# Optimization experiments

Hardware: AMD Instinct MI355X
Metric: run time of the kernel (lower is better)

Reference implementation:

```python
import jax, jax.numpy as jnp
import numpy as np

D = 48


def setup_inputs() -> dict:
    key = jax.random.key(0)
    k1, k2, k3, k4, k5 = jax.random.split(key, 5)
    B, N, d = 4, 512, D
    x = jax.random.normal(k1, (B, N, d), dtype=jnp.float32)
    # Linear(2d, 2d) and Linear(2d, d); stored as (in, out) so y = x @ W + b
    s1 = 1.0 / np.sqrt(2 * d)
    W1 = jax.random.uniform(k2, (2 * d, 2 * d), dtype=jnp.float32, minval=-s1, maxval=s1)
    b1 = jax.random.uniform(k3, (2 * d,), dtype=jnp.float32, minval=-s1, maxval=s1)
    W2 = jax.random.uniform(k4, (2 * d, d), dtype=jnp.float32, minval=-s1, maxval=s1)
    b2 = jax.random.uniform(k5, (d,), dtype=jnp.float32, minval=-s1, maxval=s1)
    return {"x": x, "W1": W1, "b1": b1, "W2": W2, "b2": b2}


def reference(x, W1, b1, W2, b2):
    B, N, d = x.shape
    # pairwise concat: [B, N, N, 2d] with (i, j) = (x_i, x_j)
    xi = jnp.broadcast_to(x[:, :, None, :], (B, N, N, d))
    xj = jnp.broadcast_to(x[:, None, :, :], (B, N, N, d))
    cat = jnp.concatenate([xi, xj], axis=-1)
    h = jax.nn.gelu(cat @ W1 + b1, approximate=False)  # torch GELU is exact erf form
    p = h @ W2 + b2  # [B, N, N, d]
    mask = jnp.triu(jnp.ones((N, N), dtype=bool), 1)  # j > i masked
    p = jnp.where(mask[None, :, :, None], 0.0, p)
    w = jnp.sqrt(jnp.sum(p * p, axis=-1))  # frobenius norm over feature dim -> [B, N, N]
    w = jnp.where(mask[None, :, :], -1e9, w)
    w = jax.nn.softmax(w, axis=-1)[..., None]  # softmax over j
    return jnp.sum(w * p, axis=2)  # [B, N, d]
```

## Files before the change

kernel.cpp:

```cpp
#include <hip/hip_runtime.h>
#include <hip/hip_bf16.h>
#include <hip/hip_fp16.h>
#include <math.h>

#define DD 48
#define NN 512
#define TWO_D 96
#define ROWS 2048
#define W2P 104

typedef __attribute__((ext_vector_type(8))) _Float16 f16x8;
typedef __attribute__((ext_vector_type(4))) float f32x4;
typedef __attribute__((ext_vector_type(2))) float f32x2;
typedef __attribute__((ext_vector_type(4))) unsigned int u32x4;

__device__ __forceinline__ __half2 h2cast(unsigned int u) { return __builtin_bit_cast(__half2, u); }

__device__ __forceinline__ f32x2 gelu_poly2(f32x2 u) {
    f32x2 lim;  lim  = 3.5777f;
    f32x2 nlim; nlim = -3.5777f;
    const f32x2 uc = __builtin_elementwise_min(__builtin_elementwise_max(u, nlim), lim);
    const f32x2 v = uc * uc;
    f32x2 c5; c5 = -1.04448e-6f;
    f32x2 c4; c4 = 4.61896e-5f;
    f32x2 c3; c3 = -8.62284e-4f;
    f32x2 c2; c2 = 9.22138e-3f;
    f32x2 c1; c1 = -6.58353e-2f;
    f32x2 c0; c0 = 3.98855e-1f;
    f32x2 E = __builtin_elementwise_fma(v, c5, c4);
    E = __builtin_elementwise_fma(v, E, c3);
    E = __builtin_elementwise_fma(v, E, c2);
    E = __builtin_elementwise_fma(v, E, c1);
    E = __builtin_elementwise_fma(v, E, c0);
    f32x2 hlf; hlf = 0.5f;
    return u * __builtin_elementwise_fma(uc, E, hlf);
}

__global__ __launch_bounds__(256) void precompute_kernel(
        const float* __restrict__ x,
        const float* __restrict__ W1,
        const float* __restrict__ b1,
        const float* __restrict__ W2,
        __half* __restrict__ Aout,
        __half* __restrict__ Bout,
        __half* __restrict__ W2T) {
    if (blockIdx.x == ROWS / 4) {
        for (int idx = threadIdx.x; idx < DD * TWO_D; idx += 256) {
            const int f = idx / TWO_D;
            const int k = idx - f * TWO_D;
            W2T[idx] = __float2half(W2[k * DD + f]);
        }
        return;
    }
    const int wave = threadIdx.x >> 6;
    const int lane = threadIdx.x & 63;
    const int row = blockIdx.x * 4 + wave;
    __shared__ float xs[4][DD];
    if (threadIdx.x < 4 * DD)
        xs[threadIdx.x / DD][threadIdx.x % DD] = x[blockIdx.x * 4 * DD + threadIdx.x];
    __syncthreads();
    for (int t = lane; t < TWO_D; t += 64) {
        float a0 = 0.f, a1 = 0.f;
#pragma unroll 8
        for (int k = 0; k < DD; ++k) {
            const float xv = xs[wave][k];
            a0 = fmaf(xv, W1[k * TWO_D + t], a0);
            a1 = fmaf(xv, W1[(DD + k) * TWO_D + t], a1);
        }
        Aout[row * TWO_D + t] = __float2half(a0 + b1[t]);
        Bout[row * TWO_D + t] = __float2half(a1);
    }
}


#define LOAD_PB(PB_, PTR_)                                                      \
  { _Pragma("unroll")                                                           \
    for (int ks = 0; ks < 3; ++ks)                                              \
      PB_[ks] = *(const u32x4*)&(PTR_)[ks * 32 + q8]; }

#define STREAM_KS(PB_, ACC_, PF_, NPTR_, KS_)                                   \
  { const u32x4 aw = avp[KS_];                                                  \
    const u32x4 bw = PB_[KS_];                                                  \
    if (PF_) PB_[KS_] = *(const u32x4*)&(NPTR_)[(KS_) * 32 + q8];               \
    const __half2 u0 = __hadd2(h2cast(aw.x), h2cast(bw.x));                     \
    const __half2 u1 = __hadd2(h2cast(aw.y), h2cast(bw.y));                     \
    const __half2 u2 = __hadd2(h2cast(aw.z), h2cast(bw.z));                     \
    const __half2 u3 = __hadd2(h2cast(aw.w), h2cast(bw.w));                     \
    f32x2 f0, f1, f2, f3;                                                       \
    { float2 t_ = __half22float2(u0); f0.x = t_.x; f0.y = t_.y; }               \
    { float2 t_ = __half22float2(u1); f1.x = t_.x; f1.y = t_.y; }               \
    { float2 t_ = __half22float2(u2); f2.x = t_.x; f2.y = t_.y; }               \
    { float2 t_ = __half22float2(u3); f3.x = t_.x; f3.y = t_.y; }               \
    const f32x2 g0 = gelu_poly2(f0);                                            \
    const f32x2 g1 = gelu_poly2(f1);                                            \
    const f32x2 g2 = gelu_poly2(f2);                                            \
    const f32x2 g3 = gelu_poly2(f3);                                            \
    union { f16x8 v; __half2 h2[4]; } hf;                                       \
    hf.h2[0] = __float22half2_rn(make_float2(g0.x, g0.y));                      \
    hf.h2[1] = __float22half2_rn(make_float2(g1.x, g1.y));                      \
    hf.h2[2] = __float22half2_rn(make_float2(g2.x, g2.y));                      \
    hf.h2[3] = __float22half2_rn(make_float2(g3.x, g3.y));                      \
    ACC_[0] = __builtin_amdgcn_mfma_f32_16x16x32_f16(bf0, hf.v, ACC_[0], 0, 0, 0); \
    ACC_[1] = __builtin_amdgcn_mfma_f32_16x16x32_f16(bf1, hf.v, ACC_[1], 0, 0, 0); \
    ACC_[2] = __builtin_amdgcn_mfma_f32_16x16x32_f16(bf2, hf.v, ACC_[2], 0, 0, 0); \
  }

#define FUSED_KS(PBa_, ACCa_, PFa_, NPa_, DOB_, PBb_, ACCb_, PFb_, NPb_)        \
  { _Pragma("unroll")                                                           \
    for (int ksi = 0; ksi < 3; ++ksi) {                                         \
      const f16x8 bf0 = *(const f16x8*)&w2s[(0 * 16 + n) * W2P + ksi * 32 + q8];\
      const f16x8 bf1 = *(const f16x8*)&w2s[(1 * 16 + n) * W2P + ksi * 32 + q8];\
      const f16x8 bf2 = *(const f16x8*)&w2s[(2 * 16 + n) * W2P + ksi * 32 + q8];\
      STREAM_KS(PBa_, ACCa_, PFa_, NPa_, ksi);                                  \
      if (DOB_) STREAM_KS(PBb_, ACCb_, PFb_, NPb_, ksi);                        \
    } }

#define CHUNK_EPI(J0_, I_, ACC_, L_, O_)                                        \
  { f32x2 pv[3][2];                                                             \
    f32x2 ss2; ss2 = 0.f;                                                       \
    _Pragma("unroll")                                                           \
    for (int t = 0; t < 3; ++t) {                                               \
      pv[t][0].x = ACC_[t][0]; pv[t][0].y = ACC_[t][1];                         \
      pv[t][1].x = ACC_[t][2]; pv[t][1].y = ACC_[t][3];                         \
      ss2 = __builtin_elementwise_fma(pv[t][0], pv[t][0], ss2);                 \
      ss2 = __builtin_elementwise_fma(pv[t][1], pv[t][1], ss2);                 \
    }                                                                           \
    float ss = ss2.x + ss2.y;                                                   \
    ss += __shfl_xor(ss, 16);                                                   \
    ss += __shfl_xor(ss, 32);                                                   \
    const int j = (J0_) + n;                                                    \
    const float ew = (j <= (I_))                                                \
        ? __builtin_amdgcn_exp2f(sqrtf(ss) * 1.44269504f) : 0.f;                \
    L_ += ew;                                                                   \
    f32x2 ew2; ew2 = ew;                                                        \
    _Pragma("unroll")                                                           \
    for (int t = 0; t < 3; ++t) {                                               \
      O_[t][0] = __builtin_elementwise_fma(ew2, pv[t][0], O_[t][0]);            \
      O_[t][1] = __builtin_elementwise_fma(ew2, pv[t][1], O_[t][1]);            \
    } }

#define ACC_INIT(ACC_)                                                          \
  { ACC_[0] = b2q[0]; ACC_[1] = b2q[1]; ACC_[2] = b2q[2]; }

#define PROCESS_ROW_DUAL(I_, ROW_, CSTART_, L_, O_)                             \
  { u32x4 avp[3];                                                               \
    _Pragma("unroll")                                                           \
    for (int ks = 0; ks < 3; ++ks)                                              \
      avp[ks] = *(const u32x4*)&Arow[(size_t)(ROW_) * TWO_D + ks * 32 + q8];    \
    const int nch = ((I_) + 16) >> 4;                                           \
    int c = (CSTART_);                                                          \
    const __half* __restrict__ Bp = Bbase + (size_t)((c << 4) + n) * TWO_D;     \
    u32x4 pbA[3], pbB[3];                                                       \
    if (c < nch) LOAD_PB(pbA, Bp);                                              \
    if (c + 4 < nch) LOAD_PB(pbB, Bp + 64 * TWO_D);                             \
    for (; c + 4 < nch; c += 8) {                                               \
      const bool pfA = (c + 8) < nch;                                           \
      const bool pfB = (c + 12) < nch;                                          \
      const __half* __restrict__ BpA = Bp + 128 * TWO_D;                        \
      const __half* __restrict__ BpB = Bp + 192 * TWO_D;                        \
      f32x4 accA[3], accB[3];                                                   \
      ACC_INIT(accA); ACC_INIT(accB);                                           \
      FUSED_KS(pbA, accA, pfA, BpA, true, pbB, accB, pfB, BpB);                 \
      CHUNK_EPI((c << 4), I_, accA, L_, O_);                                    \
      CHUNK_EPI(((c + 4) << 4), I_, accB, L_, O_);                              \
      Bp = BpA;                                                                 \
    }                                                                           \
    if (c < nch) {                                                              \
      f32x4 accA[3];                                                            \
      ACC_INIT(accA);                                                           \
      FUSED_KS(pbA, accA, false, Bp, false, pbB, accA, false, Bp);              \
      CHUNK_EPI((c << 4), I_, accA, L_, O_);                                    \
    } }

#define REDUCE_FLUSH(L_, O_, SEL_)                                              \
  { _Pragma("unroll")                                                           \
    for (int d = 1; d <= 8; d <<= 1) {                                          \
      L_ += __shfl_xor(L_, d);                                                  \
      _Pragma("unroll")                                                         \
      for (int t = 0; t < 3; ++t)                                               \
        _Pragma("unroll")                                                       \
        for (int r = 0; r < 2; ++r) {                                           \
          O_[t][r].x += __shfl_xor(O_[t][r].x, d);                              \
          O_[t][r].y += __shfl_xor(O_[t][r].y, d);                              \
        }                                                                       \
    }                                                                           \
    if (n == 0) {                                                               \
      _Pragma("unroll")                                                         \
      for (int t = 0; t < 3; ++t)                                               \
        _Pragma("unroll")                                                       \
        for (int r = 0; r < 2; ++r) {                                           \
          ored[wave][SEL_][t * 16 + 4 * q + 2 * r + 0] = O_[t][r].x;            \
          ored[wave][SEL_][t * 16 + 4 * q + 2 * r + 1] = O_[t][r].y;            \
        }                                                                       \
      if (q == 0) lred[wave][SEL_] = L_;                                        \
    } }

__global__ __launch_bounds__(256) void pair_softmax_kernel(
        const __half* __restrict__ Arow,
        const __half* __restrict__ Brow,
        const __half* __restrict__ W2T,
        const float* __restrict__ b2,
        float* __restrict__ out) {
    const int batch = blockIdx.x >> 8;
    const int pr = blockIdx.x & 255;
    const int iH = (NN - 1) - pr;
    const int iL = pr;
    const int cH = (iH >> 4) + 1;
    const int rowH = batch * NN + iH;
    const int rowL = batch * NN + iL;
    const __half* __restrict__ Bbase = Brow + (size_t)batch * NN * TWO_D;

    const int tid = threadIdx.x;
    const int wave = tid >> 6;
    const int lane = tid & 63;
    const int n = lane & 15;
    const int q = lane >> 4;
    const int q8 = q * 8;

    __shared__ __align__(16) __half w2s[DD * W2P];
    __shared__ float lred[4][2];
    __shared__ float ored[4][2][DD];

    for (int idx = tid; idx < DD * TWO_D; idx += 256) {
        const int f = idx / TWO_D;
        const int k = idx - f * TWO_D;
        w2s[f * W2P + k] = W2T[idx];
    }
    __syncthreads();

    f32x4 b2q[3];
#pragma unroll
    for (int t = 0; t < 3; ++t)
        b2q[t] = *(const f32x4*)&b2[t * 16 + 4 * q];

    float lH = 0.f;
    f32x2 oH[3][2];
#pragma unroll
    for (int t = 0; t < 3; ++t)
#pragma unroll
        for (int r = 0; r < 2; ++r) oH[t][r] = 0.f;

    PROCESS_ROW_DUAL(iH, rowH, wave, lH, oH);
    REDUCE_FLUSH(lH, oH, 0);

    float lL = 0.f;
    f32x2 oL[3][2];
#pragma unroll
    for (int t = 0; t < 3; ++t)
#pragma unroll
        for (int r = 0; r < 2; ++r) oL[t][r] = 0.f;

    const int cstartL = (wave + 128 - cH) & 3;
    PROCESS_ROW_DUAL(iL, rowL, cstartL, lL, oL);
    REDUCE_FLUSH(lL, oL, 1);

    __syncthreads();
    if (tid < 2 * DD) {
        const int sel = tid / DD;
        const int f = tid - sel * DD;
        float L = 0.f, O = 0.f;
#pragma unroll
        for (int wv = 0; wv < 4; ++wv) {
            L += lred[wv][sel];
            O += ored[wv][sel][f];
        }
        const int row = sel ? rowL : rowH;
        out[row * DD + f] = O / L;
    }
}

extern "C" void kernel_launch(void* const* d_in, const int* in_sizes, int n_in,
                              void* d_out, int out_size, void* d_ws, size_t ws_size,
                              hipStream_t stream) {
    const float* x  = (const float*)d_in[0];
    const float* W1 = (const float*)d_in[1];
    const float* b1 = (const float*)d_in[2];
    const float* W2 = (const float*)d_in[3];
    const float* b2 = (const float*)d_in[4];
    float* outp = (float*)d_out;

    __half* A   = (__half*)d_ws;
    __half* Bb  = A + ROWS * TWO_D;
    __half* W2T = Bb + ROWS * TWO_D;

    precompute_kernel<<<ROWS / 4 + 1, 256, 0, stream>>>(x, W1, b1, W2, A, Bb, W2T);
    pair_softmax_kernel<<<1024, 256, 0, stream>>>(A, Bb, W2T, b2, outp);
}
```

Baseline: 92.75 us.

## Use six waves per block with single-chunk streaming loop instead of dual-chunk

Raises the pair-softmax block from 4 to 6 waves, so each wave strides over 16-column chunks by 6. It replaces the dual-chunk interleaved loop (two accumulator sets and two prefetch buffers) with a simpler single-chunk loop that prefetches the next chunk. b2 moves into shared memory. This trades the per-wave instruction-level parallelism of the dual stream for more waves per block and lower register pressure, and changes how work is balanced across waves.

New measurement: 105.4 us. +13.6%, slower.

```diff
diff --git a/kernel.cpp b/kernel.cpp
--- a/kernel.cpp
+++ b/kernel.cpp
@@ -8,6 +8,7 @@
 #define TWO_D 96
 #define ROWS 2048
 #define W2P 104
+#define NW 6
 
 typedef __attribute__((ext_vector_type(8))) _Float16 f16x8;
 typedef __attribute__((ext_vector_type(4))) float f32x4;
@@ -72,104 +73,81 @@
     }
 }
 
-
-#define LOAD_PB(PB_, PTR_)                                                      \
-  { _Pragma("unroll")                                                           \
-    for (int ks = 0; ks < 3; ++ks)                                              \
-      PB_[ks] = *(const u32x4*)&(PTR_)[ks * 32 + q8]; }
-
-#define STREAM_KS(PB_, ACC_, PF_, NPTR_, KS_)                                   \
-  { const u32x4 aw = avp[KS_];                                                  \
-    const u32x4 bw = PB_[KS_];                                                  \
-    if (PF_) PB_[KS_] = *(const u32x4*)&(NPTR_)[(KS_) * 32 + q8];               \
-    const __half2 u0 = __hadd2(h2cast(aw.x), h2cast(bw.x));                     \
-    const __half2 u1 = __hadd2(h2cast(aw.y), h2cast(bw.y));                     \
-    const __half2 u2 = __hadd2(h2cast(aw.z), h2cast(bw.z));                     \
-    const __half2 u3 = __hadd2(h2cast(aw.w), h2cast(bw.w));                     \
-    f32x2 f0, f1, f2, f3;                                                       \
-    { float2 t_ = __half22float2(u0); f0.x = t_.x; f0.y = t_.y; }               \
-    { float2 t_ = __half22float2(u1); f1.x = t_.x; f1.y = t_.y; }               \
-    { float2 t_ = __half22float2(u2); f2.x = t_.x; f2.y = t_.y; }               \
-    { float2 t_ = __half22float2(u3); f3.x = t_.x; f3.y = t_.y; }               \
-    const f32x2 g0 = gelu_poly2(f0);                                            \
-    const f32x2 g1 = gelu_poly2(f1);                                            \
-    const f32x2 g2 = gelu_poly2(f2);                                            \
-    const f32x2 g3 = gelu_poly2(f3);                                            \
-    union { f16x8 v; __half2 h2[4]; } hf;                                       \
-    hf.h2[0] = __float22half2_rn(make_float2(g0.x, g0.y));                      \
-    hf.h2[1] = __float22half2_rn(make_float2(g1.x, g1.y));                      \
-    hf.h2[2] = __float22half2_rn(make_float2(g2.x, g2.y));                      \
-    hf.h2[3] = __float22half2_rn(make_float2(g3.x, g3.y));                      \
-    ACC_[0] = __builtin_amdgcn_mfma_f32_16x16x32_f16(bf0, hf.v, ACC_[0], 0, 0, 0); \
-    ACC_[1] = __builtin_amdgcn_mfma_f32_16x16x32_f16(bf1, hf.v, ACC_[1], 0, 0, 0); \
-    ACC_[2] = __builtin_amdgcn_mfma_f32_16x16x32_f16(bf2, hf.v, ACC_[2], 0, 0, 0); \
-  }
-
-#define FUSED_KS(PBa_, ACCa_, PFa_, NPa_, DOB_, PBb_, ACCb_, PFb_, NPb_)        \
-  { _Pragma("unroll")                                                           \
-    for (int ksi = 0; ksi < 3; ++ksi) {                                         \
-      const f16x8 bf0 = *(const f16x8*)&w2s[(0 * 16 + n) * W2P + ksi * 32 + q8];\
-      const f16x8 bf1 = *(const f16x8*)&w2s[(1 * 16 + n) * W2P + ksi * 32 + q8];\
-      const f16x8 bf2 = *(const f16x8*)&w2s[(2 * 16 + n) * W2P + ksi * 32 + q8];\
-      STREAM_KS(PBa_, ACCa_, PFa_, NPa_, ksi);                                  \
-      if (DOB_) STREAM_KS(PBb_, ACCb_, PFb_, NPb_, ksi);                        \
-    } }
-
-#define CHUNK_EPI(J0_, I_, ACC_, L_, O_)                                        \
-  { f32x2 pv[3][2];                                                             \
-    f32x2 ss2; ss2 = 0.f;                                                       \
-    _Pragma("unroll")                                                           \
-    for (int t = 0; t < 3; ++t) {                                               \
-      pv[t][0].x = ACC_[t][0]; pv[t][0].y = ACC_[t][1];                         \
-      pv[t][1].x = ACC_[t][2]; pv[t][1].y = ACC_[t][3];                         \
-      ss2 = __builtin_elementwise_fma(pv[t][0], pv[t][0], ss2);                 \
-      ss2 = __builtin_elementwise_fma(pv[t][1], pv[t][1], ss2);                 \
-    }                                                                           \
-    float ss = ss2.x + ss2.y;                                                   \
-    ss += __shfl_xor(ss, 16);                                                   \
-    ss += __shfl_xor(ss, 32);                                                   \
-    const int j = (J0_) + n;                                                    \
-    const float ew = (j <= (I_))                                                \
-        ? __builtin_amdgcn_exp2f(sqrtf(ss) * 1.44269504f) : 0.f;                \
-    L_ += ew;                                                                   \
-    f32x2 ew2; ew2 = ew;                                                        \
-    _Pragma("unroll")                                                           \
-    for (int t = 0; t < 3; ++t) {                                               \
-      O_[t][0] = __builtin_elementwise_fma(ew2, pv[t][0], O_[t][0]);            \
-      O_[t][1] = __builtin_elementwise_fma(ew2, pv[t][1], O_[t][1]);            \
-    } }
-
-#define ACC_INIT(ACC_)                                                          \
-  { ACC_[0] = b2q[0]; ACC_[1] = b2q[1]; ACC_[2] = b2q[2]; }
-
-#define PROCESS_ROW_DUAL(I_, ROW_, CSTART_, L_, O_)                             \
+#define PROCESS_ROW_S(I_, ROW_, CSTART_, L_, O_)                                \
   { u32x4 avp[3];                                                               \
     _Pragma("unroll")                                                           \
     for (int ks = 0; ks < 3; ++ks)                                              \
       avp[ks] = *(const u32x4*)&Arow[(size_t)(ROW_) * TWO_D + ks * 32 + q8];    \
     const int nch = ((I_) + 16) >> 4;                                           \
     int c = (CSTART_);                                                          \
-    const __half* __restrict__ Bp = Bbase + (size_t)((c << 4) + n) * TWO_D;     \
-    u32x4 pbA[3], pbB[3];                                                       \
-    if (c < nch) LOAD_PB(pbA, Bp);                                              \
-    if (c + 4 < nch) LOAD_PB(pbB, Bp + 64 * TWO_D);                             \
-    for (; c + 4 < nch; c += 8) {                                               \
-      const bool pfA = (c + 8) < nch;                                           \
-      const bool pfB = (c + 12) < nch;                                          \
-      const __half* __restrict__ BpA = Bp + 128 * TWO_D;                        \
-      const __half* __restrict__ BpB = Bp + 192 * TWO_D;                        \
-      f32x4 accA[3], accB[3];                                                   \
-      ACC_INIT(accA); ACC_INIT(accB);                                           \
-      FUSED_KS(pbA, accA, pfA, BpA, true, pbB, accB, pfB, BpB);                 \
-      CHUNK_EPI((c << 4), I_, accA, L_, O_);                                    \
-      CHUNK_EPI(((c + 4) << 4), I_, accB, L_, O_);                              \
-      Bp = BpA;                                                                 \
-    }                                                                           \
     if (c < nch) {                                                              \
-      f32x4 accA[3];                                                            \
-      ACC_INIT(accA);                                                           \
-      FUSED_KS(pbA, accA, false, Bp, false, pbB, accA, false, Bp);              \
-      CHUNK_EPI((c << 4), I_, accA, L_, O_);                                    \
+      const __half* __restrict__ Bp = Bbase + (size_t)((c << 4) + n) * TWO_D;   \
+      u32x4 pb[3];                                                              \
+      _Pragma("unroll")                                                         \
+      for (int ks = 0; ks < 3; ++ks)                                            \
+        pb[ks] = *(const u32x4*)&Bp[ks * 32 + q8];                              \
+      for (; c < nch; c += NW) {                                                \
+        const __half* __restrict__ Bn =                                         \
+            ((c + NW) < nch) ? Bp + (NW * 16) * TWO_D : Bp;        \
+        f32x4 acc[3];                                                           \
+        acc[0] = *(const f32x4*)&b2s[0 * 16 + 4 * q];                           \
+        acc[1] = *(const f32x4*)&b2s[1 * 16 + 4 * q];                           \
+        acc[2] = *(const f32x4*)&b2s[2 * 16 + 4 * q];                           \
+        _Pragma("unroll")                                                       \
+        for (int ks = 0; ks < 3; ++ks) {                                        \
+          const f16x8 bf0 = *(const f16x8*)&w2s[(0 * 16 + n) * W2P + ks * 32 + q8]; \
+          const f16x8 bf1 = *(const f16x8*)&w2s[(1 * 16 + n) * W2P + ks * 32 + q8]; \
+          const f16x8 bf2 = *(const f16x8*)&w2s[(2 * 16 + n) * W2P + ks * 32 + q8]; \
+          const u32x4 aw = avp[ks];                                             \
+          const u32x4 bw = pb[ks];                                              \
+          pb[ks] = *(const u32x4*)&Bn[ks * 32 + q8];                            \
+          const __half2 u0 = __hadd2(h2cast(aw.x), h2cast(bw.x));               \
+          const __half2 u1 = __hadd2(h2cast(aw.y), h2cast(bw.y));               \
+          const __half2 u2 = __hadd2(h2cast(aw.z), h2cast(bw.z));               \
+          const __half2 u3 = __hadd2(h2cast(aw.w), h2cast(bw.w));               \
+          f32x2 f0, f1, f2, f3;                                                 \
+          { float2 t_ = __half22float2(u0); f0.x = t_.x; f0.y = t_.y; }         \
+          { float2 t_ = __half22float2(u1); f1.x = t_.x; f1.y = t_.y; }         \
+          { float2 t_ = __half22float2(u2); f2.x = t_.x; f2.y = t_.y; }         \
+          { float2 t_ = __half22float2(u3); f3.x = t_.x; f3.y = t_.y; }         \
+          const f32x2 g0 = gelu_poly2(f0);                                      \
+          const f32x2 g1 = gelu_poly2(f1);                                      \
+          const f32x2 g2 = gelu_poly2(f2);                                      \
+          const f32x2 g3 = gelu_poly2(f3);                                      \
+          union { f16x8 v; __half2 h2[4]; } hf;                                 \
+          hf.h2[0] = __float22half2_rn(make_float2(g0.x, g0.y));                \
+          hf.h2[1] = __float22half2_rn(make_float2(g1.x, g1.y));                \
+          hf.h2[2] = __float22half2_rn(make_float2(g2.x, g2.y));                \
+          hf.h2[3] = __float22half2_rn(make_float2(g3.x, g3.y));                \
+          acc[0] = __builtin_amdgcn_mfma_f32_16x16x32_f16(bf0, hf.v, acc[0], 0, 0, 0); \
+          acc[1] = __builtin_amdgcn_mfma_f32_16x16x32_f16(bf1, hf.v, acc[1], 0, 0, 0); \
+          acc[2] = __builtin_amdgcn_mfma_f32_16x16x32_f16(bf2, hf.v, acc[2], 0, 0, 0); \
+        }                                                                       \
+        \
+        f32x2 pv[3][2];                                                         \
+        f32x2 ss2; ss2 = 0.f;                                                   \
+        _Pragma("unroll")                                                       \
+        for (int t = 0; t < 3; ++t) {                                           \
+          pv[t][0].x = acc[t][0]; pv[t][0].y = acc[t][1];                       \
+          pv[t][1].x = acc[t][2]; pv[t][1].y = acc[t][3];                       \
+          ss2 = __builtin_elementwise_fma(pv[t][0], pv[t][0], ss2);             \
+          ss2 = __builtin_elementwise_fma(pv[t][1], pv[t][1], ss2);             \
+        }                                                                       \
+        float ss = ss2.x + ss2.y;                                               \
+        ss += __shfl_xor(ss, 16);                                               \
+        ss += __shfl_xor(ss, 32);                                               \
+        const int j = (c << 4) + n;                                             \
+        const float ew = (j <= (I_))                                            \
+            ? __builtin_amdgcn_exp2f(sqrtf(ss) * 1.44269504f) : 0.f;            \
+        L_ += ew;                                                               \
+        f32x2 ew2; ew2 = ew;                                                    \
+        _Pragma("unroll")                                                       \
+        for (int t = 0; t < 3; ++t) {                                           \
+          O_[t][0] = __builtin_elementwise_fma(ew2, pv[t][0], O_[t][0]);        \
+          O_[t][1] = __builtin_elementwise_fma(ew2, pv[t][1], O_[t][1]);        \
+        }                                                                       \
+        Bp = Bn;                                                                \
+      }                                                                         \
     } }
 
 #define REDUCE_FLUSH(L_, O_, SEL_)                                              \
@@ -195,7 +173,7 @@
       if (q == 0) lred[wave][SEL_] = L_;                                        \
     } }
 
-__global__ __launch_bounds__(256) void pair_softmax_kernel(
+__global__ __launch_bounds__(384) void pair_softmax_kernel(
         const __half* __restrict__ Arow,
         const __half* __restrict__ Brow,
         const __half* __restrict__ W2T,
@@ -218,20 +196,20 @@
     const int q8 = q * 8;
 
     __shared__ __align__(16) __half w2s[DD * W2P];
-    __shared__ float lred[4][2];
-    __shared__ float ored[4][2][DD];
-
-    for (int idx = tid; idx < DD * TWO_D; idx += 256) {
+    __shared__ __align__(16) float b2s[DD];
+    __shared__ float lred[NW][2];
+    __shared__ float ored[NW][2][DD];
+
+    for (int idx = tid; idx < DD * TWO_D; idx += 384) {
         const int f = idx / TWO_D;
         const int k = idx - f * TWO_D;
         w2s[f * W2P + k] = W2T[idx];
     }
+    if (tid < DD) b2s[tid] = b2[tid];
     __syncthreads();
 
-    f32x4 b2q[3];
-#pragma unroll
-    for (int t = 0; t < 3; ++t)
-        b2q[t] = *(const f32x4*)&b2[t * 16 + 4 * q];
+    int cstartL = (wave - cH) % NW;
+    if (cstartL < 0) cstartL += NW;
 
     float lH = 0.f;
     f32x2 oH[3][2];
@@ -239,8 +217,7 @@
     for (int t = 0; t < 3; ++t)
 #pragma unroll
         for (int r = 0; r < 2; ++r) oH[t][r] = 0.f;
-
-    PROCESS_ROW_DUAL(iH, rowH, wave, lH, oH);
+    PROCESS_ROW_S(iH, rowH, wave, lH, oH);
     REDUCE_FLUSH(lH, oH, 0);
 
     float lL = 0.f;
@@ -249,9 +226,7 @@
     for (int t = 0; t < 3; ++t)
 #pragma unroll
         for (int r = 0; r < 2; ++r) oL[t][r] = 0.f;
-
-    const int cstartL = (wave + 128 - cH) & 3;
-    PROCESS_ROW_DUAL(iL, rowL, cstartL, lL, oL);
+    PROCESS_ROW_S(iL, rowL, cstartL, lL, oL);
     REDUCE_FLUSH(lL, oL, 1);
 
     __syncthreads();
@@ -260,7 +235,7 @@
         const int f = tid - sel * DD;
         float L = 0.f, O = 0.f;
 #pragma unroll
-        for (int wv = 0; wv < 4; ++wv) {
+        for (int wv = 0; wv < NW; ++wv) {
             L += lred[wv][sel];
             O += ored[wv][sel][f];
         }
@@ -284,5 +259,5 @@
     __half* W2T = Bb + ROWS * TWO_D;
 
     precompute_kernel<<<ROWS / 4 + 1, 256, 0, stream>>>(x, W1, b1, W2, A, Bb, W2T);
-    pair_softmax_kernel<<<1024, 256, 0, stream>>>(A, Bb, W2T, b2, outp);
-}
+    pair_softmax_kernel<<<1024, 384, 0, stream>>>(A, Bb, W2T, b2, outp);
+}
```
